# Optimization experiments

Hardware: AMD Instinct MI355X
Metric: run time of the kernel (lower is better)

The kernel has to match this reference:

```python
import jax, jax.numpy as jnp
import numpy as np

N_NODES = 100000
N_EDGES = 1600000
D_FEAT = 128
N_CLASSES = 2
K_HOPS = 2


def setup_inputs() -> dict:
    key = jax.random.key(0)
    k1, k2, k3, k4 = jax.random.split(key, 4)
    x = jax.random.normal(k1, (N_NODES, D_FEAT), dtype=jnp.float32)
    edge_index = jax.random.randint(k2, (2, N_EDGES), 0, N_NODES, dtype=jnp.int64)
    weight = jax.random.normal(k3, (N_CLASSES, D_FEAT), dtype=jnp.float32) * (1.0 / np.sqrt(D_FEAT))
    bias = jnp.zeros((N_CLASSES,), dtype=jnp.float32)
    return {"x": x, "edge_index": edge_index, "weight": weight, "bias": bias}


def reference(x, edge_index, weight, bias):
    N = x.shape[0]
    # gcn_norm with self-loops (PyG SGConv default)
    loop = jnp.arange(N, dtype=edge_index.dtype)
    row = jnp.concatenate([edge_index[0], loop])  # source nodes
    col = jnp.concatenate([edge_index[1], loop])  # target nodes
    ones = jnp.ones(row.shape[0], dtype=x.dtype)
    deg = jax.ops.segment_sum(ones, col, num_segments=N)
    dinv = jnp.where(deg > 0, jax.lax.rsqrt(deg), 0.0)
    norm = dinv[row] * dinv[col]  # [E+N]

    # K hops of normalized sparse propagation: x <- A_norm @ x
    for _ in range(K_HOPS):
        x = jax.ops.segment_sum(x[row] * norm[:, None], col, num_segments=N)

    logits = x @ weight.T + bias  # [N, num_classes]
    return jax.nn.log_softmax(logits, axis=1)
```

## Files before the change

kernel.cpp:

```cpp
#include <hip/hip_runtime.h>

#define D_FEAT 128
#define BSH    8
#define BNODES 256
#define MAXNB  400
#define NSEG   512
#define SEGCAP 16
#define SENT   0xFFFFFFFFu
#define OVCAP  (1u << 20)

__global__ __launch_bounds__(256) void k_matvec(const float* __restrict__ x,
                                                const float* __restrict__ w,
                                                float2* __restrict__ z, int n) {
    int wave = (int)((blockIdx.x * blockDim.x + threadIdx.x) >> 6);
    int lane = threadIdx.x & 63;
    if (wave >= n) return;
    const float2 xv = *(const float2*)(x + (size_t)wave * D_FEAT + 2 * lane);
    const float2 w0 = *(const float2*)(w + 2 * lane);
    const float2 w1 = *(const float2*)(w + D_FEAT + 2 * lane);
    float p0 = xv.x * w0.x + xv.y * w0.y;
    float p1 = xv.x * w1.x + xv.y * w1.y;
    #pragma unroll
    for (int off = 32; off > 0; off >>= 1) {
        p0 += __shfl_down(p0, off, 64);
        p1 += __shfl_down(p1, off, 64);
    }
    if (lane == 0) z[wave] = make_float2(p0, p1);
}

__global__ __launch_bounds__(256) void k_bucket(const int* __restrict__ row,
                                                const int* __restrict__ col,
                                                unsigned* __restrict__ ovcnt,
                                                unsigned long long* __restrict__ ovbuf,
                                                unsigned* __restrict__ gbuf,
                                                int E, int NB) {
    __shared__ unsigned lcnt[MAXNB];
    __shared__ unsigned lbuf[MAXNB * SEGCAP];
    const int tid = threadIdx.x;
    for (int i = tid; i < NB; i += 256) lcnt[i] = 0;
    __syncthreads();

    const int chunk = (E + NSEG - 1) / NSEG;
    const int s = blockIdx.x * chunk;
    const int e_end = min(s + chunk, E);
    for (int e = s + tid; e < e_end; e += 256) {
        int r = row[e], c = col[e];
        int b = c >> BSH;
        unsigned pos = atomicAdd(&lcnt[b], 1u);
        if (pos < SEGCAP) {
            lbuf[b * SEGCAP + pos] = ((unsigned)r << BSH) | (unsigned)(c & (BNODES - 1));
        } else {
            unsigned gi = atomicAdd(ovcnt, 1u);
            if (gi < OVCAP)
                ovbuf[gi] = ((unsigned long long)(unsigned)r << 32) | (unsigned)c;
        }
    }
    __syncthreads();

    const unsigned blk = blockIdx.x;
    const int total = NB * SEGCAP;
    for (int idx = tid; idx < total; idx += 256) {
        int b = idx >> 4;
        int slot = idx & 15;
        unsigned cnt = lcnt[b]; if (cnt > SEGCAP) cnt = SEGCAP;
        unsigned v = ((unsigned)slot < cnt) ? lbuf[idx] : SENT;
        gbuf[((size_t)b * NSEG + blk) * SEGCAP + slot] = v;
    }
}

__global__ __launch_bounds__(256) void k_degdinv(const unsigned* __restrict__ gbuf,
                                                 const unsigned* __restrict__ ovcnt,
                                                 const unsigned long long* __restrict__ ovbuf,
                                                 const float2* __restrict__ z,
                                                 float* __restrict__ dinv,
                                                 float2* __restrict__ zd, int n) {
    __shared__ unsigned hist[BNODES];
    const int b = blockIdx.x, tid = threadIdx.x;
    hist[tid] = 0;
    __syncthreads();
    const unsigned* p = gbuf + (size_t)b * NSEG * SEGCAP;
    for (int i = tid; i < NSEG * SEGCAP; i += 256) {
        unsigned v = p[i];
        if (v != SENT) atomicAdd(&hist[v & (BNODES - 1)], 1u);
    }
    unsigned oc = *ovcnt; if (oc > OVCAP) oc = OVCAP;
    for (unsigned i = tid; i < oc; i += 256) {
        unsigned long long e = ovbuf[i];
        unsigned c = (unsigned)e;
        if ((int)(c >> BSH) == b) atomicAdd(&hist[c & (BNODES - 1)], 1u);
    }
    __syncthreads();
    int c = (b << BSH) + tid;
    if (c < n) {
        float d = rsqrtf((float)hist[tid] + 1.0f);
        dinv[c] = d;
        float2 zc = z[c];
        zd[c] = make_float2(zc.x * d, zc.y * d);
    }
}

__global__ __launch_bounds__(256) void k_hop_mid(const unsigned* __restrict__ gbuf,
                                                 const unsigned* __restrict__ ovcnt,
                                                 const unsigned long long* __restrict__ ovbuf,
                                                 const float* __restrict__ dinv,
                                                 const float2* __restrict__ vd,
                                                 float2* __restrict__ out_vd, int n) {
    __shared__ float accx[BNODES];
    __shared__ float accy[BNODES];
    const int b = blockIdx.x, tid = threadIdx.x;
    accx[tid] = 0.0f; accy[tid] = 0.0f;
    __syncthreads();
    const unsigned* p = gbuf + (size_t)b * NSEG * SEGCAP;
    for (int i = tid; i < NSEG * SEGCAP; i += 256) {
        unsigned v = p[i];
        if (v != SENT) {
            float2 vv = vd[v >> BSH];
            int cl = (int)(v & (BNODES - 1));
            atomicAdd(&accx[cl], vv.x);
            atomicAdd(&accy[cl], vv.y);
        }
    }
    unsigned oc = *ovcnt; if (oc > OVCAP) oc = OVCAP;
    for (unsigned i = tid; i < oc; i += 256) {
        unsigned long long e = ovbuf[i];
        unsigned c = (unsigned)e;
        if ((int)(c >> BSH) == b) {
            float2 vv = vd[(unsigned)(e >> 32)];
            int cl = (int)(c & (BNODES - 1));
            atomicAdd(&accx[cl], vv.x);
            atomicAdd(&accy[cl], vv.y);
        }
    }
    __syncthreads();
    int c = (b << BSH) + tid;
    if (c < n) {
        float d = dinv[c];
        float dd = d * d;
        float2 s = vd[c];
        out_vd[c] = make_float2((s.x + accx[tid]) * dd, (s.y + accy[tid]) * dd);
    }
}

__global__ __launch_bounds__(256) void k_hop_final(const unsigned* __restrict__ gbuf,
                                                   const unsigned* __restrict__ ovcnt,
                                                   const unsigned long long* __restrict__ ovbuf,
                                                   const float* __restrict__ dinv,
                                                   const float2* __restrict__ vd,
                                                   const float* __restrict__ bias,
                                                   float2* __restrict__ out, int n) {
    __shared__ float accx[BNODES];
    __shared__ float accy[BNODES];
    const int b = blockIdx.x, tid = threadIdx.x;
    accx[tid] = 0.0f; accy[tid] = 0.0f;
    __syncthreads();
    const unsigned* p = gbuf + (size_t)b * NSEG * SEGCAP;
    for (int i = tid; i < NSEG * SEGCAP; i += 256) {
        unsigned v = p[i];
        if (v != SENT) {
            float2 vv = vd[v >> BSH];
            int cl = (int)(v & (BNODES - 1));
            atomicAdd(&accx[cl], vv.x);
            atomicAdd(&accy[cl], vv.y);
        }
    }
    unsigned oc = *ovcnt; if (oc > OVCAP) oc = OVCAP;
    for (unsigned i = tid; i < oc; i += 256) {
        unsigned long long e = ovbuf[i];
        unsigned c = (unsigned)e;
        if ((int)(c >> BSH) == b) {
            float2 vv = vd[(unsigned)(e >> 32)];
            int cl = (int)(c & (BNODES - 1));
            atomicAdd(&accx[cl], vv.x);
            atomicAdd(&accy[cl], vv.y);
        }
    }
    __syncthreads();
    int c = (b << BSH) + tid;
    if (c < n) {
        float d = dinv[c];
        float2 s = vd[c];
        float l0 = (s.x + accx[tid]) * d + bias[0];
        float l1 = (s.y + accy[tid]) * d + bias[1];
        float mx = fmaxf(l0, l1);
        float lse = mx + logf(expf(l0 - mx) + expf(l1 - mx));
        out[c] = make_float2(l0 - lse, l1 - lse);
    }
}


__global__ __launch_bounds__(256) void k_deg(const int* __restrict__ col,
                                             unsigned int* __restrict__ deg, int E) {
    int e = blockIdx.x * blockDim.x + threadIdx.x;
    if (e < E) atomicAdd(&deg[col[e]], 1u);
}

__global__ __launch_bounds__(256) void k_dinv_init(const unsigned int* __restrict__ deg,
                                                   float* __restrict__ dinv,
                                                   const float2* __restrict__ zin,
                                                   float2* __restrict__ yout, int n) {
    int i = blockIdx.x * blockDim.x + threadIdx.x;
    if (i < n) {
        float d = rsqrtf((float)deg[i] + 1.0f);
        dinv[i] = d;
        float2 zi = zin[i];
        float dd = d * d;
        yout[i] = make_float2(zi.x * dd, zi.y * dd);
    }
}

__global__ __launch_bounds__(256) void k_selfloop(const float* __restrict__ dinv,
                                                  const float2* __restrict__ zin,
                                                  float2* __restrict__ yout, int n) {
    int i = blockIdx.x * blockDim.x + threadIdx.x;
    if (i < n) {
        float d = dinv[i];
        float dd = d * d;
        float2 zi = zin[i];
        yout[i] = make_float2(zi.x * dd, zi.y * dd);
    }
}

__global__ __launch_bounds__(256) void k_edge(const int* __restrict__ row,
                                              const int* __restrict__ col,
                                              const float* __restrict__ dinv,
                                              const float2* __restrict__ zin,
                                              float* __restrict__ yout, int E) {
    int e = blockIdx.x * blockDim.x + threadIdx.x;
    if (e < E) {
        int r = row[e], c = col[e];
        float nr = dinv[r] * dinv[c];
        float2 zr = zin[r];
        atomicAdd(&yout[2 * c + 0], zr.x * nr);
        atomicAdd(&yout[2 * c + 1], zr.y * nr);
    }
}

__global__ __launch_bounds__(256) void k_final(const float2* __restrict__ y,
                                               const float* __restrict__ bias,
                                               float2* __restrict__ out, int n) {
    int i = blockIdx.x * blockDim.x + threadIdx.x;
    if (i < n) {
        float2 l = y[i];
        float l0 = l.x + bias[0];
        float l1 = l.y + bias[1];
        float m = fmaxf(l0, l1);
        float lse = m + logf(expf(l0 - m) + expf(l1 - m));
        out[i] = make_float2(l0 - lse, l1 - lse);
    }
}

extern "C" void kernel_launch(void* const* d_in, const int* in_sizes, int n_in,
                              void* d_out, int out_size, void* d_ws, size_t ws_size,
                              hipStream_t stream) {
    const float* x    = (const float*)d_in[0];
    const int*   ei   = (const int*)d_in[1];
    const float* w    = (const float*)d_in[2];
    const float* bias = (const float*)d_in[3];

    const int n = in_sizes[0] / D_FEAT;
    const int E = in_sizes[1] / 2;
    const int* row = ei;
    const int* col = ei + E;

    const int TB = 256;
    const int nodeBlocks = (n + TB - 1) / TB;
    const int edgeBlocks = (E + TB - 1) / TB;
    const int waveBlocks = (n + 3) / 4;

    const int NB = (n + BNODES - 1) >> BSH;

    size_t needSeg = 128
                   + (size_t)OVCAP * 8
                   + (size_t)NB * NSEG * SEGCAP * 4
                   + (size_t)n * (3 * sizeof(float2) + sizeof(float));

    if (NB <= MAXNB && n < (1 << 24) && ws_size >= needSeg) {
        char* ws = (char*)d_ws;
        unsigned* ovcnt = (unsigned*)ws;              ws += 128;
        unsigned long long* ovbuf = (unsigned long long*)ws; ws += (size_t)OVCAP * 8;
        unsigned* gbuf = (unsigned*)ws;               ws += (size_t)NB * NSEG * SEGCAP * 4;
        float2* z    = (float2*)ws;                   ws += (size_t)n * sizeof(float2);
        float2* zd   = (float2*)ws;                   ws += (size_t)n * sizeof(float2);
        float2* y1d  = (float2*)ws;                   ws += (size_t)n * sizeof(float2);
        float*  dinv = (float*)ws;

        hipMemsetAsync(ovcnt, 0, 128, stream);
        k_bucket<<<NSEG, TB, 0, stream>>>(row, col, ovcnt, ovbuf, gbuf, E, NB);
        k_matvec<<<waveBlocks, TB, 0, stream>>>(x, w, z, n);
        k_degdinv<<<NB, TB, 0, stream>>>(gbuf, ovcnt, ovbuf, z, dinv, zd, n);
        k_hop_mid<<<NB, TB, 0, stream>>>(gbuf, ovcnt, ovbuf, dinv, zd, y1d, n);
        k_hop_final<<<NB, TB, 0, stream>>>(gbuf, ovcnt, ovbuf, dinv, y1d, bias,
                                           (float2*)d_out, n);
    } else {
        char* ws = (char*)d_ws;
        float2* z   = (float2*)ws; ws += (size_t)n * sizeof(float2);
        float2* y1  = (float2*)ws; ws += (size_t)n * sizeof(float2);
        float2* y2  = (float2*)ws; ws += (size_t)n * sizeof(float2);
        float*  dinv = (float*)ws; ws += (size_t)n * sizeof(float);
        unsigned int* deg = (unsigned int*)ws;

        hipMemsetAsync(deg, 0, (size_t)n * sizeof(unsigned int), stream);
        k_deg<<<edgeBlocks, TB, 0, stream>>>(col, deg, E);
        k_matvec<<<waveBlocks, TB, 0, stream>>>(x, w, z, n);
        k_dinv_init<<<nodeBlocks, TB, 0, stream>>>(deg, dinv, z, y1, n);
        k_edge<<<edgeBlocks, TB, 0, stream>>>(row, col, dinv, z, (float*)y1, E);
        k_selfloop<<<nodeBlocks, TB, 0, stream>>>(dinv, y1, y2, n);
        k_edge<<<edgeBlocks, TB, 0, stream>>>(row, col, dinv, y1, (float*)y2, E);
        k_final<<<nodeBlocks, TB, 0, stream>>>(y2, bias, (float2*)d_out, n);
    }
}
```

Measured before the change: 183.7 us.

## Split per-bucket aggregation across four blocks with separate reduce kernels

```diff
diff --git a/kernel.cpp b/kernel.cpp
--- a/kernel.cpp
+++ b/kernel.cpp
@@ -8,6 +8,8 @@
 #define SEGCAP 16
 #define SENT   0xFFFFFFFFu
 #define OVCAP  (1u << 20)
+#define SPLIT  4
+#define SEGPS  (NSEG / SPLIT)
 
 __global__ __launch_bounds__(256) void k_matvec(const float* __restrict__ x,
                                                 const float* __restrict__ w,
@@ -68,123 +70,121 @@
     }
 }
 
-__global__ __launch_bounds__(256) void k_degdinv(const unsigned* __restrict__ gbuf,
-                                                 const unsigned* __restrict__ ovcnt,
-                                                 const unsigned long long* __restrict__ ovbuf,
-                                                 const float2* __restrict__ z,
-                                                 float* __restrict__ dinv,
-                                                 float2* __restrict__ zd, int n) {
+__global__ __launch_bounds__(256) void k_deg_part(const unsigned* __restrict__ gbuf,
+                                                  const unsigned* __restrict__ ovcnt,
+                                                  const unsigned long long* __restrict__ ovbuf,
+                                                  unsigned* __restrict__ pdeg) {
     __shared__ unsigned hist[BNODES];
-    const int b = blockIdx.x, tid = threadIdx.x;
+    const int b = blockIdx.x >> 2, s = blockIdx.x & 3, tid = threadIdx.x;
     hist[tid] = 0;
     __syncthreads();
-    const unsigned* p = gbuf + (size_t)b * NSEG * SEGCAP;
-    for (int i = tid; i < NSEG * SEGCAP; i += 256) {
-        unsigned v = p[i];
-        if (v != SENT) atomicAdd(&hist[v & (BNODES - 1)], 1u);
-    }
-    unsigned oc = *ovcnt; if (oc > OVCAP) oc = OVCAP;
-    for (unsigned i = tid; i < oc; i += 256) {
-        unsigned long long e = ovbuf[i];
-        unsigned c = (unsigned)e;
-        if ((int)(c >> BSH) == b) atomicAdd(&hist[c & (BNODES - 1)], 1u);
-    }
-    __syncthreads();
-    int c = (b << BSH) + tid;
-    if (c < n) {
-        float d = rsqrtf((float)hist[tid] + 1.0f);
-        dinv[c] = d;
-        float2 zc = z[c];
-        zd[c] = make_float2(zc.x * d, zc.y * d);
-    }
-}
-
-__global__ __launch_bounds__(256) void k_hop_mid(const unsigned* __restrict__ gbuf,
-                                                 const unsigned* __restrict__ ovcnt,
-                                                 const unsigned long long* __restrict__ ovbuf,
-                                                 const float* __restrict__ dinv,
-                                                 const float2* __restrict__ vd,
-                                                 float2* __restrict__ out_vd, int n) {
+    const uint4* p4 = (const uint4*)(gbuf + ((size_t)b * NSEG + (size_t)s * SEGPS) * SEGCAP);
+    for (int j = tid; j < SEGPS * SEGCAP / 4; j += 256) {
+        uint4 v = p4[j];
+        if (v.x != SENT) atomicAdd(&hist[v.x & (BNODES - 1)], 1u);
+        if (v.y != SENT) atomicAdd(&hist[v.y & (BNODES - 1)], 1u);
+        if (v.z != SENT) atomicAdd(&hist[v.z & (BNODES - 1)], 1u);
+        if (v.w != SENT) atomicAdd(&hist[v.w & (BNODES - 1)], 1u);
+    }
+    if (s == 0) {
+        unsigned oc = *ovcnt; if (oc > OVCAP) oc = OVCAP;
+        for (unsigned i = tid; i < oc; i += 256) {
+            unsigned c = (unsigned)ovbuf[i];
+            if ((int)(c >> BSH) == b) atomicAdd(&hist[c & (BNODES - 1)], 1u);
+        }
+    }
+    __syncthreads();
+    pdeg[(size_t)blockIdx.x * BNODES + tid] = hist[tid];
+}
+
+__global__ __launch_bounds__(256) void k_deg_reduce(const unsigned* __restrict__ pdeg,
+                                                    const float2* __restrict__ z,
+                                                    float* __restrict__ dinv,
+                                                    float2* __restrict__ zd, int n) {
+    int i = blockIdx.x * blockDim.x + threadIdx.x;
+    if (i >= n) return;
+    int b = i >> BSH, t = i & (BNODES - 1);
+    unsigned deg = 0;
+    #pragma unroll
+    for (int s = 0; s < SPLIT; ++s) deg += pdeg[(size_t)(b * SPLIT + s) * BNODES + t];
+    float d = rsqrtf((float)deg + 1.0f);
+    dinv[i] = d;
+    float2 zc = z[i];
+    zd[i] = make_float2(zc.x * d, zc.y * d);
+}
+
+__global__ __launch_bounds__(256) void k_hop_part(const unsigned* __restrict__ gbuf,
+                                                  const unsigned* __restrict__ ovcnt,
+                                                  const unsigned long long* __restrict__ ovbuf,
+                                                  const float2* __restrict__ vd,
+                                                  float2* __restrict__ pbuf) {
     __shared__ float accx[BNODES];
     __shared__ float accy[BNODES];
-    const int b = blockIdx.x, tid = threadIdx.x;
+    const int b = blockIdx.x >> 2, s = blockIdx.x & 3, tid = threadIdx.x;
     accx[tid] = 0.0f; accy[tid] = 0.0f;
     __syncthreads();
-    const unsigned* p = gbuf + (size_t)b * NSEG * SEGCAP;
-    for (int i = tid; i < NSEG * SEGCAP; i += 256) {
-        unsigned v = p[i];
-        if (v != SENT) {
-            float2 vv = vd[v >> BSH];
-            int cl = (int)(v & (BNODES - 1));
-            atomicAdd(&accx[cl], vv.x);
-            atomicAdd(&accy[cl], vv.y);
+    const uint4* p4 = (const uint4*)(gbuf + ((size_t)b * NSEG + (size_t)s * SEGPS) * SEGCAP);
+    for (int j = tid; j < SEGPS * SEGCAP / 4; j += 256) {
+        uint4 v = p4[j];
+        if (v.x != SENT) { float2 t = vd[v.x >> BSH]; int c = v.x & (BNODES-1); atomicAdd(&accx[c], t.x); atomicAdd(&accy[c], t.y); }
+        if (v.y != SENT) { float2 t = vd[v.y >> BSH]; int c = v.y & (BNODES-1); atomicAdd(&accx[c], t.x); atomicAdd(&accy[c], t.y); }
+        if (v.z != SENT) { float2 t = vd[v.z >> BSH]; int c = v.z & (BNODES-1); atomicAdd(&accx[c], t.x); atomicAdd(&accy[c], t.y); }
+        if (v.w != SENT) { float2 t = vd[v.w >> BSH]; int c = v.w & (BNODES-1); atomicAdd(&accx[c], t.x); atomicAdd(&accy[c], t.y); }
+    }
+    if (s == 0) {
+        unsigned oc = *ovcnt; if (oc > OVCAP) oc = OVCAP;
+        for (unsigned i = tid; i < oc; i += 256) {
+            unsigned long long e = ovbuf[i];
+            unsigned c = (unsigned)e;
+            if ((int)(c >> BSH) == b) {
+                float2 t = vd[(unsigned)(e >> 32)];
+                int cl = (int)(c & (BNODES - 1));
+                atomicAdd(&accx[cl], t.x);
+                atomicAdd(&accy[cl], t.y);
+            }
         }
     }
-    unsigned oc = *ovcnt; if (oc > OVCAP) oc = OVCAP;
-    for (unsigned i = tid; i < oc; i += 256) {
-        unsigned long long e = ovbuf[i];
-        unsigned c = (unsigned)e;
-        if ((int)(c >> BSH) == b) {
-            float2 vv = vd[(unsigned)(e >> 32)];
-            int cl = (int)(c & (BNODES - 1));
-            atomicAdd(&accx[cl], vv.x);
-            atomicAdd(&accy[cl], vv.y);
-        }
-    }
-    __syncthreads();
-    int c = (b << BSH) + tid;
-    if (c < n) {
-        float d = dinv[c];
-        float dd = d * d;
-        float2 s = vd[c];
-        out_vd[c] = make_float2((s.x + accx[tid]) * dd, (s.y + accy[tid]) * dd);
-    }
-}
-
-__global__ __launch_bounds__(256) void k_hop_final(const unsigned* __restrict__ gbuf,
-                                                   const unsigned* __restrict__ ovcnt,
-                                                   const unsigned long long* __restrict__ ovbuf,
-                                                   const float* __restrict__ dinv,
-                                                   const float2* __restrict__ vd,
-                                                   const float* __restrict__ bias,
-                                                   float2* __restrict__ out, int n) {
-    __shared__ float accx[BNODES];
-    __shared__ float accy[BNODES];
-    const int b = blockIdx.x, tid = threadIdx.x;
-    accx[tid] = 0.0f; accy[tid] = 0.0f;
-    __syncthreads();
-    const unsigned* p = gbuf + (size_t)b * NSEG * SEGCAP;
-    for (int i = tid; i < NSEG * SEGCAP; i += 256) {
-        unsigned v = p[i];
-        if (v != SENT) {
-            float2 vv = vd[v >> BSH];
-            int cl = (int)(v & (BNODES - 1));
-            atomicAdd(&accx[cl], vv.x);
-            atomicAdd(&accy[cl], vv.y);
-        }
-    }
-    unsigned oc = *ovcnt; if (oc > OVCAP) oc = OVCAP;
-    for (unsigned i = tid; i < oc; i += 256) {
-        unsigned long long e = ovbuf[i];
-        unsigned c = (unsigned)e;
-        if ((int)(c >> BSH) == b) {
-            float2 vv = vd[(unsigned)(e >> 32)];
-            int cl = (int)(c & (BNODES - 1));
-            atomicAdd(&accx[cl], vv.x);
-            atomicAdd(&accy[cl], vv.y);
-        }
-    }
-    __syncthreads();
-    int c = (b << BSH) + tid;
-    if (c < n) {
-        float d = dinv[c];
-        float2 s = vd[c];
-        float l0 = (s.x + accx[tid]) * d + bias[0];
-        float l1 = (s.y + accy[tid]) * d + bias[1];
-        float mx = fmaxf(l0, l1);
-        float lse = mx + logf(expf(l0 - mx) + expf(l1 - mx));
-        out[c] = make_float2(l0 - lse, l1 - lse);
-    }
+    __syncthreads();
+    pbuf[(size_t)blockIdx.x * BNODES + tid] = make_float2(accx[tid], accy[tid]);
+}
+
+__global__ __launch_bounds__(256) void k_mid_reduce(const float2* __restrict__ pbuf,
+                                                    const float2* __restrict__ vd,
+                                                    const float* __restrict__ dinv,
+                                                    float2* __restrict__ out_vd, int n) {
+    int i = blockIdx.x * blockDim.x + threadIdx.x;
+    if (i >= n) return;
+    int b = i >> BSH, t = i & (BNODES - 1);
+    float2 acc = vd[i];
+    #pragma unroll
+    for (int s = 0; s < SPLIT; ++s) {
+        float2 p = pbuf[(size_t)(b * SPLIT + s) * BNODES + t];
+        acc.x += p.x; acc.y += p.y;
+    }
+    float d = dinv[i], dd = d * d;
+    out_vd[i] = make_float2(acc.x * dd, acc.y * dd);
+}
+
+__global__ __launch_bounds__(256) void k_fin_reduce(const float2* __restrict__ pbuf,
+                                                    const float2* __restrict__ vd,
+                                                    const float* __restrict__ dinv,
+                                                    const float* __restrict__ bias,
+                                                    float2* __restrict__ out, int n) {
+    int i = blockIdx.x * blockDim.x + threadIdx.x;
+    if (i >= n) return;
+    int b = i >> BSH, t = i & (BNODES - 1);
+    float2 acc = vd[i];
+    #pragma unroll
+    for (int s = 0; s < SPLIT; ++s) {
+        float2 p = pbuf[(size_t)(b * SPLIT + s) * BNODES + t];
+        acc.x += p.x; acc.y += p.y;
+    }
+    float d = dinv[i];
+    float l0 = acc.x * d + bias[0];
+    float l1 = acc.y * d + bias[1];
+    float mx = fmaxf(l0, l1);
+    float lse = mx + logf(expf(l0 - mx) + expf(l1 - mx));
+    out[i] = make_float2(l0 - lse, l1 - lse);
 }
 
 
@@ -272,7 +272,9 @@
     size_t needSeg = 128
                    + (size_t)OVCAP * 8
                    + (size_t)NB * NSEG * SEGCAP * 4
-                   + (size_t)n * (3 * sizeof(float2) + sizeof(float));
+                   + (size_t)n * (3 * sizeof(float2) + sizeof(float))
+                   + (size_t)NB * SPLIT * BNODES * sizeof(float2)
+                   + (size_t)NB * SPLIT * BNODES * sizeof(unsigned);
 
     if (NB <= MAXNB && n < (1 << 24) && ws_size >= needSeg) {
         char* ws = (char*)d_ws;
@@ -282,15 +284,20 @@
         float2* z    = (float2*)ws;                   ws += (size_t)n * sizeof(float2);
         float2* zd   = (float2*)ws;                   ws += (size_t)n * sizeof(float2);
         float2* y1d  = (float2*)ws;                   ws += (size_t)n * sizeof(float2);
-        float*  dinv = (float*)ws;
+        float*  dinv = (float*)ws;                    ws += (size_t)n * sizeof(float);
+        float2* pbuf = (float2*)ws;                   ws += (size_t)NB * SPLIT * BNODES * sizeof(float2);
+        unsigned* pdeg = (unsigned*)ws;
 
         hipMemsetAsync(ovcnt, 0, 128, stream);
         k_bucket<<<NSEG, TB, 0, stream>>>(row, col, ovcnt, ovbuf, gbuf, E, NB);
         k_matvec<<<waveBlocks, TB, 0, stream>>>(x, w, z, n);
-        k_degdinv<<<NB, TB, 0, stream>>>(gbuf, ovcnt, ovbuf, z, dinv, zd, n);
-        k_hop_mid<<<NB, TB, 0, stream>>>(gbuf, ovcnt, ovbuf, dinv, zd, y1d, n);
-        k_hop_final<<<NB, TB, 0, stream>>>(gbuf, ovcnt, ovbuf, dinv, y1d, bias,
-                                           (float2*)d_out, n);
+        k_deg_part<<<NB * SPLIT, TB, 0, stream>>>(gbuf, ovcnt, ovbuf, pdeg);
+        k_deg_reduce<<<nodeBlocks, TB, 0, stream>>>(pdeg, z, dinv, zd, n);
+        k_hop_part<<<NB * SPLIT, TB, 0, stream>>>(gbuf, ovcnt, ovbuf, zd, pbuf);
+        k_mid_reduce<<<nodeBlocks, TB, 0, stream>>>(pbuf, zd, dinv, y1d, n);
+        k_hop_part<<<NB * SPLIT, TB, 0, stream>>>(gbuf, ovcnt, ovbuf, y1d, pbuf);
+        k_fin_reduce<<<nodeBlocks, TB, 0, stream>>>(pbuf, y1d, dinv, bias,
+                                                    (float2*)d_out, n);
     } else {
         char* ws = (char*)d_ws;
         float2* z   = (float2*)ws; ws += (size_t)n * sizeof(float2);
```

After: 179.8 us. -2.1%, faster.

## Build per-bucket CSR once and run hops as node-parallel gathers

Applied to the files above, without the earlier changes.

```diff
diff --git a/kernel.cpp b/kernel.cpp
--- a/kernel.cpp
+++ b/kernel.cpp
@@ -4,10 +4,11 @@
 #define BSH    8
 #define BNODES 256
 #define MAXNB  400
-#define NSEG   512
-#define SEGCAP 16
+#define NSEG   1024
+#define SEGCAP 8
 #define SENT   0xFFFFFFFFu
-#define OVCAP  (1u << 20)
+#define OVCAP  (1u << 18)
+#define BUCKCAP 5120
 
 __global__ __launch_bounds__(256) void k_matvec(const float* __restrict__ x,
                                                 const float* __restrict__ w,
@@ -60,130 +61,137 @@
     const unsigned blk = blockIdx.x;
     const int total = NB * SEGCAP;
     for (int idx = tid; idx < total; idx += 256) {
-        int b = idx >> 4;
-        int slot = idx & 15;
+        int b = idx >> 3;
+        int slot = idx & 7;
         unsigned cnt = lcnt[b]; if (cnt > SEGCAP) cnt = SEGCAP;
         unsigned v = ((unsigned)slot < cnt) ? lbuf[idx] : SENT;
         gbuf[((size_t)b * NSEG + blk) * SEGCAP + slot] = v;
     }
 }
 
-__global__ __launch_bounds__(256) void k_degdinv(const unsigned* __restrict__ gbuf,
-                                                 const unsigned* __restrict__ ovcnt,
-                                                 const unsigned long long* __restrict__ ovbuf,
-                                                 const float2* __restrict__ z,
-                                                 float* __restrict__ dinv,
-                                                 float2* __restrict__ zd, int n) {
+__global__ __launch_bounds__(256) void k_csr(const unsigned* __restrict__ gbuf,
+                                             const unsigned* __restrict__ ovcnt,
+                                             const unsigned long long* __restrict__ ovbuf,
+                                             const float2* __restrict__ z,
+                                             int* __restrict__ csr,
+                                             int2* __restrict__ meta,
+                                             float* __restrict__ dinv,
+                                             float2* __restrict__ zd, int n) {
     __shared__ unsigned hist[BNODES];
+    __shared__ unsigned sstart[BNODES];
+    __shared__ unsigned tmp[BNODES];
     const int b = blockIdx.x, tid = threadIdx.x;
     hist[tid] = 0;
     __syncthreads();
-    const unsigned* p = gbuf + (size_t)b * NSEG * SEGCAP;
-    for (int i = tid; i < NSEG * SEGCAP; i += 256) {
-        unsigned v = p[i];
-        if (v != SENT) atomicAdd(&hist[v & (BNODES - 1)], 1u);
+
+    const uint4* p4 = (const uint4*)(gbuf + (size_t)b * NSEG * SEGCAP);
+    const int n4 = NSEG * SEGCAP / 4;
+    for (int j = tid; j < n4; j += 256) {
+        uint4 v = p4[j];
+        if (v.x != SENT) atomicAdd(&hist[v.x & (BNODES - 1)], 1u);
+        if (v.y != SENT) atomicAdd(&hist[v.y & (BNODES - 1)], 1u);
+        if (v.z != SENT) atomicAdd(&hist[v.z & (BNODES - 1)], 1u);
+        if (v.w != SENT) atomicAdd(&hist[v.w & (BNODES - 1)], 1u);
     }
     unsigned oc = *ovcnt; if (oc > OVCAP) oc = OVCAP;
     for (unsigned i = tid; i < oc; i += 256) {
-        unsigned long long e = ovbuf[i];
-        unsigned c = (unsigned)e;
+        unsigned c = (unsigned)ovbuf[i];
         if ((int)(c >> BSH) == b) atomicAdd(&hist[c & (BNODES - 1)], 1u);
     }
     __syncthreads();
+
+    unsigned myc = hist[tid];
+    tmp[tid] = myc;
+    __syncthreads();
+    unsigned val = myc;
+    #pragma unroll
+    for (int off = 1; off < 256; off <<= 1) {
+        unsigned add = (tid >= off) ? tmp[tid - off] : 0u;
+        __syncthreads();
+        val += add;
+        tmp[tid] = val;
+        __syncthreads();
+    }
+    unsigned excl = val - myc;
+    sstart[tid] = excl;
+
     int c = (b << BSH) + tid;
     if (c < n) {
-        float d = rsqrtf((float)hist[tid] + 1.0f);
+        meta[c] = make_int2(b * BUCKCAP + (int)excl, (int)myc);
+        float d = rsqrtf((float)myc + 1.0f);
         dinv[c] = d;
         float2 zc = z[c];
         zd[c] = make_float2(zc.x * d, zc.y * d);
     }
-}
-
-__global__ __launch_bounds__(256) void k_hop_mid(const unsigned* __restrict__ gbuf,
-                                                 const unsigned* __restrict__ ovcnt,
-                                                 const unsigned long long* __restrict__ ovbuf,
-                                                 const float* __restrict__ dinv,
-                                                 const float2* __restrict__ vd,
-                                                 float2* __restrict__ out_vd, int n) {
-    __shared__ float accx[BNODES];
-    __shared__ float accy[BNODES];
-    const int b = blockIdx.x, tid = threadIdx.x;
-    accx[tid] = 0.0f; accy[tid] = 0.0f;
-    __syncthreads();
-    const unsigned* p = gbuf + (size_t)b * NSEG * SEGCAP;
-    for (int i = tid; i < NSEG * SEGCAP; i += 256) {
-        unsigned v = p[i];
-        if (v != SENT) {
-            float2 vv = vd[v >> BSH];
-            int cl = (int)(v & (BNODES - 1));
-            atomicAdd(&accx[cl], vv.x);
-            atomicAdd(&accy[cl], vv.y);
-        }
-    }
-    unsigned oc = *ovcnt; if (oc > OVCAP) oc = OVCAP;
+    hist[tid] = excl;
+    __syncthreads();
+
+    int* dst = csr + (size_t)b * BUCKCAP;
+    for (int j = tid; j < n4; j += 256) {
+        uint4 v = p4[j];
+        if (v.x != SENT) { unsigned p = atomicAdd(&hist[v.x & (BNODES-1)], 1u); if (p < BUCKCAP) dst[p] = (int)(v.x >> BSH); }
+        if (v.y != SENT) { unsigned p = atomicAdd(&hist[v.y & (BNODES-1)], 1u); if (p < BUCKCAP) dst[p] = (int)(v.y >> BSH); }
+        if (v.z != SENT) { unsigned p = atomicAdd(&hist[v.z & (BNODES-1)], 1u); if (p < BUCKCAP) dst[p] = (int)(v.z >> BSH); }
+        if (v.w != SENT) { unsigned p = atomicAdd(&hist[v.w & (BNODES-1)], 1u); if (p < BUCKCAP) dst[p] = (int)(v.w >> BSH); }
+    }
     for (unsigned i = tid; i < oc; i += 256) {
         unsigned long long e = ovbuf[i];
-        unsigned c = (unsigned)e;
-        if ((int)(c >> BSH) == b) {
-            float2 vv = vd[(unsigned)(e >> 32)];
-            int cl = (int)(c & (BNODES - 1));
-            atomicAdd(&accx[cl], vv.x);
-            atomicAdd(&accy[cl], vv.y);
+        unsigned cc = (unsigned)e;
+        if ((int)(cc >> BSH) == b) {
+            unsigned p = atomicAdd(&hist[cc & (BNODES - 1)], 1u);
+            if (p < BUCKCAP) dst[p] = (int)(e >> 32);
         }
     }
-    __syncthreads();
-    int c = (b << BSH) + tid;
-    if (c < n) {
-        float d = dinv[c];
-        float dd = d * d;
-        float2 s = vd[c];
-        out_vd[c] = make_float2((s.x + accx[tid]) * dd, (s.y + accy[tid]) * dd);
-    }
-}
-
-__global__ __launch_bounds__(256) void k_hop_final(const unsigned* __restrict__ gbuf,
-                                                   const unsigned* __restrict__ ovcnt,
-                                                   const unsigned long long* __restrict__ ovbuf,
-                                                   const float* __restrict__ dinv,
-                                                   const float2* __restrict__ vd,
-                                                   const float* __restrict__ bias,
-                                                   float2* __restrict__ out, int n) {
-    __shared__ float accx[BNODES];
-    __shared__ float accy[BNODES];
-    const int b = blockIdx.x, tid = threadIdx.x;
-    accx[tid] = 0.0f; accy[tid] = 0.0f;
-    __syncthreads();
-    const unsigned* p = gbuf + (size_t)b * NSEG * SEGCAP;
-    for (int i = tid; i < NSEG * SEGCAP; i += 256) {
-        unsigned v = p[i];
-        if (v != SENT) {
-            float2 vv = vd[v >> BSH];
-            int cl = (int)(v & (BNODES - 1));
-            atomicAdd(&accx[cl], vv.x);
-            atomicAdd(&accy[cl], vv.y);
-        }
-    }
-    unsigned oc = *ovcnt; if (oc > OVCAP) oc = OVCAP;
-    for (unsigned i = tid; i < oc; i += 256) {
-        unsigned long long e = ovbuf[i];
-        unsigned c = (unsigned)e;
-        if ((int)(c >> BSH) == b) {
-            float2 vv = vd[(unsigned)(e >> 32)];
-            int cl = (int)(c & (BNODES - 1));
-            atomicAdd(&accx[cl], vv.x);
-            atomicAdd(&accy[cl], vv.y);
-        }
-    }
-    __syncthreads();
-    int c = (b << BSH) + tid;
-    if (c < n) {
-        float d = dinv[c];
-        float2 s = vd[c];
-        float l0 = (s.x + accx[tid]) * d + bias[0];
-        float l1 = (s.y + accy[tid]) * d + bias[1];
+}
+
+__global__ __launch_bounds__(256) void k_hop1(const int2* __restrict__ meta,
+                                              const int* __restrict__ csr,
+                                              const float* __restrict__ dinv,
+                                              const float2* __restrict__ zd,
+                                              float2* __restrict__ y1d, int n) {
+    int gtid = blockIdx.x * blockDim.x + threadIdx.x;
+    int node = gtid >> 2, sub = gtid & 3;
+    if (node >= n) return;
+    int2 m = meta[node];
+    float ax = 0.f, ay = 0.f;
+    for (int j = sub; j < m.y; j += 4) {
+        float2 v = zd[csr[m.x + j]];
+        ax += v.x; ay += v.y;
+    }
+    ax += __shfl_xor(ax, 1, 64); ay += __shfl_xor(ay, 1, 64);
+    ax += __shfl_xor(ax, 2, 64); ay += __shfl_xor(ay, 2, 64);
+    if (sub == 0) {
+        float d = dinv[node], dd = d * d;
+        float2 s = zd[node];
+        y1d[node] = make_float2((s.x + ax) * dd, (s.y + ay) * dd);
+    }
+}
+
+__global__ __launch_bounds__(256) void k_hop2(const int2* __restrict__ meta,
+                                              const int* __restrict__ csr,
+                                              const float* __restrict__ dinv,
+                                              const float2* __restrict__ y1d,
+                                              const float* __restrict__ bias,
+                                              float2* __restrict__ out, int n) {
+    int gtid = blockIdx.x * blockDim.x + threadIdx.x;
+    int node = gtid >> 2, sub = gtid & 3;
+    if (node >= n) return;
+    int2 m = meta[node];
+    float ax = 0.f, ay = 0.f;
+    for (int j = sub; j < m.y; j += 4) {
+        float2 v = y1d[csr[m.x + j]];
+        ax += v.x; ay += v.y;
+    }
+    ax += __shfl_xor(ax, 1, 64); ay += __shfl_xor(ay, 1, 64);
+    ax += __shfl_xor(ax, 2, 64); ay += __shfl_xor(ay, 2, 64);
+    if (sub == 0) {
+        float d = dinv[node];
+        float2 s = y1d[node];
+        float l0 = (s.x + ax) * d + bias[0];
+        float l1 = (s.y + ay) * d + bias[1];
         float mx = fmaxf(l0, l1);
         float lse = mx + logf(expf(l0 - mx) + expf(l1 - mx));
-        out[c] = make_float2(l0 - lse, l1 - lse);
+        out[node] = make_float2(l0 - lse, l1 - lse);
     }
 }
 
@@ -266,31 +274,36 @@
     const int nodeBlocks = (n + TB - 1) / TB;
     const int edgeBlocks = (E + TB - 1) / TB;
     const int waveBlocks = (n + 3) / 4;
+    const int hopBlocks  = (4 * n + TB - 1) / TB;
 
     const int NB = (n + BNODES - 1) >> BSH;
 
     size_t needSeg = 128
                    + (size_t)OVCAP * 8
                    + (size_t)NB * NSEG * SEGCAP * 4
+                   + (size_t)NB * BUCKCAP * 4
+                   + (size_t)n * sizeof(int2)
                    + (size_t)n * (3 * sizeof(float2) + sizeof(float));
 
     if (NB <= MAXNB && n < (1 << 24) && ws_size >= needSeg) {
         char* ws = (char*)d_ws;
-        unsigned* ovcnt = (unsigned*)ws;              ws += 128;
+        unsigned* ovcnt = (unsigned*)ws;                     ws += 128;
         unsigned long long* ovbuf = (unsigned long long*)ws; ws += (size_t)OVCAP * 8;
-        unsigned* gbuf = (unsigned*)ws;               ws += (size_t)NB * NSEG * SEGCAP * 4;
-        float2* z    = (float2*)ws;                   ws += (size_t)n * sizeof(float2);
-        float2* zd   = (float2*)ws;                   ws += (size_t)n * sizeof(float2);
-        float2* y1d  = (float2*)ws;                   ws += (size_t)n * sizeof(float2);
+        unsigned* gbuf = (unsigned*)ws;                      ws += (size_t)NB * NSEG * SEGCAP * 4;
+        int* csr       = (int*)ws;                           ws += (size_t)NB * BUCKCAP * 4;
+        int2* meta     = (int2*)ws;                          ws += (size_t)n * sizeof(int2);
+        float2* z    = (float2*)ws;                          ws += (size_t)n * sizeof(float2);
+        float2* zd   = (float2*)ws;                          ws += (size_t)n * sizeof(float2);
+        float2* y1d  = (float2*)ws;                          ws += (size_t)n * sizeof(float2);
         float*  dinv = (float*)ws;
 
         hipMemsetAsync(ovcnt, 0, 128, stream);
         k_bucket<<<NSEG, TB, 0, stream>>>(row, col, ovcnt, ovbuf, gbuf, E, NB);
         k_matvec<<<waveBlocks, TB, 0, stream>>>(x, w, z, n);
-        k_degdinv<<<NB, TB, 0, stream>>>(gbuf, ovcnt, ovbuf, z, dinv, zd, n);
-        k_hop_mid<<<NB, TB, 0, stream>>>(gbuf, ovcnt, ovbuf, dinv, zd, y1d, n);
-        k_hop_final<<<NB, TB, 0, stream>>>(gbuf, ovcnt, ovbuf, dinv, y1d, bias,
-                                           (float2*)d_out, n);
+        k_csr<<<NB, TB, 0, stream>>>(gbuf, ovcnt, ovbuf, z, csr, meta, dinv, zd, n);
+        k_hop1<<<hopBlocks, TB, 0, stream>>>(meta, csr, dinv, zd, y1d, n);
+        k_hop2<<<hopBlocks, TB, 0, stream>>>(meta, csr, dinv, y1d, bias,
+                                             (float2*)d_out, n);
     } else {
         char* ws = (char*)d_ws;
         float2* z   = (float2*)ws; ws += (size_t)n * sizeof(float2);
```

After: 247.8 us. 1.35x slower.
